# Optimization experiments

Hardware: AMD Instinct MI355X
Metric: run time of the kernel (lower is better)

The kernel has to match this reference:

```python
import jax, jax.numpy as jnp
import numpy as np
from jax import lax

DELTA = 5.0
SCALES = (10.0, 10.0, 10.0)


def _cdiff(v, axis, delta):
    # central difference along `axis` with replicate (edge) padding; output
    # boundary values are discarded later by the interior slice, so the pad
    # mode does not affect the final loss.
    axis = axis % v.ndim
    pad = [(0, 0)] * v.ndim
    pad[axis] = (1, 1)
    vp = jnp.pad(v, pad, mode='edge')
    hi = tuple(slice(2, None) if i == axis else slice(None) for i in range(v.ndim))
    lo = tuple(slice(0, -2) if i == axis else slice(None) for i in range(v.ndim))
    return (vp[hi] - vp[lo]) / (2.0 * delta)


def _vorticity(vel, delta):
    # vel: [N,3,D,H,W] with (u,v,w); x=-1, y=-2, z=-3
    u, v, w = vel[:, 0], vel[:, 1], vel[:, 2]
    vor_x = _cdiff(w, -2, delta) - _cdiff(v, -3, delta)  # dw/dy - dv/dz
    vor_y = _cdiff(u, -3, delta) - _cdiff(w, -1, delta)  # du/dz - dw/dx
    vor_z = _cdiff(v, -1, delta) - _cdiff(u, -2, delta)  # dv/dx - du/dy
    return jnp.stack([vor_x, vor_y, vor_z], axis=1)


def _mask_near_build_wall(building):
    # building: [N,1,D,H,W] binary. 3x3x3 box filter == windowed sum.
    is_in_build = 1.0 - building
    filt = lax.reduce_window(is_in_build, 0.0, lax.add,
                             (1, 1, 3, 3, 3), (1, 1, 1, 1, 1), 'SAME')
    filt = (filt > 0).astype(building.dtype)
    return ((filt * building) > 0).astype(building.dtype)


def _masked_vorticity(bs, preds, scales, delta):
    scl = jnp.asarray(scales, dtype=preds.dtype)
    vel = scl[None, :, None, None, None] * preds[:, 1:]
    omega = _vorticity(vel, delta)
    near = _mask_near_build_wall(bs)
    omega = omega[..., 1:-1, 1:-1, 1:-1]
    b = bs[..., 1:-1, 1:-1, 1:-1]
    nw = near[..., 1:-1, 1:-1, 1:-1]
    omega = omega * b * (1.0 - nw)
    num_grids = jnp.sum(b) - jnp.sum(nw)
    return omega, num_grids


def _safe_norm_ch(d):
    # 2-norm over channel dim with zero (not NaN) grad at d == 0.
    sq = jnp.sum(d * d, axis=1, keepdims=True)
    nz = sq > 0
    return jnp.where(nz, jnp.sqrt(jnp.where(nz, sq, 1.0)), 0.0)


def setup_inputs() -> dict:
    key = jax.random.key(0)
    k1, k2, k3 = jax.random.split(key, 3)
    B, C, D, H, W = 2, 4, 64, 256, 256
    predicts = jax.random.normal(k1, (B, C, D, H, W), dtype=jnp.float32)
    targets = jax.random.normal(k2, (B, C, D, H, W), dtype=jnp.float32)
    masks = jax.random.bernoulli(k3, 0.9, (B, 1, D, H, W)).astype(jnp.float32)
    return {"predicts": predicts, "targets": targets, "masks": masks}


def reference(predicts, targets, masks):
    pred, n1 = _masked_vorticity(masks, predicts, SCALES, DELTA)
    trgt, n2 = _masked_vorticity(masks, targets, SCALES, DELTA)
    diff = _safe_norm_ch(pred - trgt)
    return jnp.sum(diff) / n1
```

## Files before the change

kernel.cpp:

```cpp
#include <hip/hip_runtime.h>


#define SD 65536LL
#define SC 4194304LL

__global__ __launch_bounds__(256) void vort_dense(
    const float* __restrict__ preds, const float* __restrict__ targs,
    const float* __restrict__ masks, double* __restrict__ acc, int slot_mask)
{
    const int lane = threadIdx.x & 63;
    const int wv   = threadIdx.x >> 6;
    int blk = blockIdx.x;
    const int tile = blk & 63; blk >>= 6;
    const int d = blk % 62 + 1; blk /= 62;
    const int b = blk;
    const int h = 1 + tile * 4 + wv;
    const int w0 = lane << 2;

    float norm = 0.0f, cnt = 0.0f;

    if (h <= 254) {
        const long long mbase = (long long)b * SC + (long long)d * SD
                              + (long long)h * 256 + w0;
        const long long b1 = ((long long)(b * 4 + 1) * 64 + d) * SD
                           + (long long)h * 256 + w0;
        const long long b2 = b1 + SC;
        const long long b3 = b2 + SC;

        long long voff[10];
        voff[0] = b1 - SD;  voff[1] = b1 + SD;
        voff[2] = b1 - 256; voff[3] = b1 + 256;
        voff[4] = b2 - SD;  voff[5] = b2 + SD;
        voff[6] = b2;
        voff[7] = b3 - 256; voff[8] = b3 + 256;
        voff[9] = b3;

        float4 P[10], T[10], Mv[9];
        #pragma unroll
        for (int i = 0; i < 10; ++i) P[i] = *(const float4*)(preds + voff[i]);
        #pragma unroll
        for (int i = 0; i < 10; ++i) T[i] = *(const float4*)(targs + voff[i]);
        #pragma unroll
        for (int r = 0; r < 9; ++r) {
            const int dd = r / 3 - 1, dh = r % 3 - 1;
            Mv[r] = *(const float4*)(masks + mbase + (long long)dd * SD
                                     + (long long)dh * 256);
        }

        float Df[10][4];
        #pragma unroll
        for (int i = 0; i < 10; ++i) {
            Df[i][0] = P[i].x - T[i].x; Df[i][1] = P[i].y - T[i].y;
            Df[i][2] = P[i].z - T[i].z; Df[i][3] = P[i].w - T[i].w;
        }
        float4 M = Mv[0];
        #pragma unroll
        for (int r = 1; r < 9; ++r) {
            M.x = fminf(M.x, Mv[r].x); M.y = fminf(M.y, Mv[r].y);
            M.z = fminf(M.z, Mv[r].z); M.w = fminf(M.w, Mv[r].w);
        }

        const float vL = __shfl_up(Df[6][3], 1, 64);
        const float vR = __shfl_down(Df[6][0], 1, 64);
        const float wL = __shfl_up(Df[9][3], 1, 64);
        const float wR = __shfl_down(Df[9][0], 1, 64);
        const float ML = __shfl_up(M.w, 1, 64);
        const float MR = __shfl_down(M.x, 1, 64);

        const float vv[6] = { vL, Df[6][0], Df[6][1], Df[6][2], Df[6][3], vR };
        const float ww[6] = { wL, Df[9][0], Df[9][1], Df[9][2], Df[9][3], wR };
        const float Mm[6] = { ML, M.x, M.y, M.z, M.w, MR };

        #pragma unroll
        for (int j = 0; j < 4; ++j) {
            const int wc = w0 + j;
            const float keepv = fminf(fminf(Mm[j], Mm[j + 1]), Mm[j + 2]);
            const bool valid = (wc >= 1) && (wc <= 254) && (keepv > 0.5f);
            const float wx = (Df[8][j] - Df[7][j]) - (Df[5][j] - Df[4][j]);
            const float wy = (Df[1][j] - Df[0][j]) - (ww[j + 2] - ww[j]);
            const float wz = (vv[j + 2] - vv[j]) - (Df[3][j] - Df[2][j]);
            const float n = sqrtf(wx * wx + wy * wy + wz * wz);
            norm += valid ? n : 0.0f;
            cnt  += valid ? 1.0f : 0.0f;
        }
    }

    #pragma unroll
    for (int off = 32; off > 0; off >>= 1) {
        norm += __shfl_down(norm, off, 64);
        cnt  += __shfl_down(cnt,  off, 64);
    }
    __shared__ float ssum[4], scnt[4];
    if (lane == 0) { ssum[wv] = norm; scnt[wv] = cnt; }
    __syncthreads();
    if (threadIdx.x == 0) {
        const float s = ssum[0] + ssum[1] + ssum[2] + ssum[3];
        const float c = scnt[0] + scnt[1] + scnt[2] + scnt[3];
        double* slot = acc + 2 * (blockIdx.x & slot_mask);
        atomicAdd(&slot[0], (double)s);
        atomicAdd(&slot[1], (double)c);
    }
}

__global__ __launch_bounds__(256) void finalize_kernel(
    const double* __restrict__ acc, float* __restrict__ out, int nslots)
{
    const int lane = threadIdx.x & 63;
    const int wv   = threadIdx.x >> 6;
    double s = 0.0, c = 0.0;
    for (int i = threadIdx.x; i < nslots; i += 256) {
        s += acc[2 * i];
        c += acc[2 * i + 1];
    }
    #pragma unroll
    for (int off = 32; off > 0; off >>= 1) {
        s += __shfl_down(s, off, 64);
        c += __shfl_down(c, off, 64);
    }
    __shared__ double ss[4], sc[4];
    if (lane == 0) { ss[wv] = s; sc[wv] = c; }
    __syncthreads();
    if (threadIdx.x == 0) {
        const double S = ss[0] + ss[1] + ss[2] + ss[3];
        const double C = sc[0] + sc[1] + sc[2] + sc[3];
        out[0] = (C != 0.0) ? (float)(S / C) : 0.0f;
    }
}

extern "C" void kernel_launch(void* const* d_in, const int* in_sizes, int n_in,
                              void* d_out, int out_size, void* d_ws, size_t ws_size,
                              hipStream_t stream)
{
    const float* preds = (const float*)d_in[0];
    const float* targs = (const float*)d_in[1];
    const float* masks = (const float*)d_in[2];
    float* out = (float*)d_out;
    double* acc = (double*)d_ws;

    int nslots = 256;
    while ((size_t)nslots * 2 * sizeof(double) > ws_size && nslots > 1)
        nslots >>= 1;

    hipMemsetAsync(d_ws, 0, (size_t)nslots * 2 * sizeof(double), stream);

    const int nblocks = 2 * 62 * 64;
    vort_dense<<<nblocks, 256, 0, stream>>>(preds, targs, masks, acc,
                                            nslots - 1);
    finalize_kernel<<<1, 256, 0, stream>>>(acc, out, nslots);
}
```

Baseline: 295.5 us.

## March along depth per thread with rolling registers for z-neighbors and masks

Result: faster. 286.8 us (-3.0%).

```diff
diff --git a/kernel.cpp b/kernel.cpp
--- a/kernel.cpp
+++ b/kernel.cpp
@@ -4,7 +4,16 @@
 #define SD 65536LL
 #define SC 4194304LL
 
-__global__ __launch_bounds__(256) void vort_dense(
+__device__ __forceinline__ float4 sub4(float4 a, float4 b) {
+    return make_float4(a.x - b.x, a.y - b.y, a.z - b.z, a.w - b.w);
+}
+__device__ __forceinline__ float4 min4(float4 a, float4 b) {
+    return make_float4(fminf(a.x, b.x), fminf(a.y, b.y),
+                       fminf(a.z, b.z), fminf(a.w, b.w));
+}
+#define C4(v, j) ((j) == 0 ? (v).x : (j) == 1 ? (v).y : (j) == 2 ? (v).z : (v).w)
+
+__global__ __launch_bounds__(256) void vort_march(
     const float* __restrict__ preds, const float* __restrict__ targs,
     const float* __restrict__ masks, double* __restrict__ acc, int slot_mask)
 {
@@ -12,76 +21,100 @@
     const int wv   = threadIdx.x >> 6;
     int blk = blockIdx.x;
     const int tile = blk & 63; blk >>= 6;
-    const int d = blk % 62 + 1; blk /= 62;
-    const int b = blk;
+    const int c    = blk & 15; blk >>= 4;
+    const int b    = blk;
+    const int d0   = 1 + 4 * c;
+    const int nstep = (c < 15) ? 4 : 2;
     const int h = 1 + tile * 4 + wv;
     const int w0 = lane << 2;
 
     float norm = 0.0f, cnt = 0.0f;
 
     if (h <= 254) {
-        const long long mbase = (long long)b * SC + (long long)d * SD
-                              + (long long)h * 256 + w0;
-        const long long b1 = ((long long)(b * 4 + 1) * 64 + d) * SD
-                           + (long long)h * 256 + w0;
-        const long long b2 = b1 + SC;
-        const long long b3 = b2 + SC;
+        const long long rowhw = (long long)h * 256 + w0;
+        const long long mrow  = (long long)b * SC + (long long)d0 * SD + rowhw;
+        const long long urow  = ((long long)(b * 4 + 1) * 64 + d0) * SD + rowhw;
+        const long long vrow  = urow + SC;
+        const long long wrow  = vrow + SC;
 
-        long long voff[10];
-        voff[0] = b1 - SD;  voff[1] = b1 + SD;
-        voff[2] = b1 - 256; voff[3] = b1 + 256;
-        voff[4] = b2 - SD;  voff[5] = b2 + SD;
-        voff[6] = b2;
-        voff[7] = b3 - 256; voff[8] = b3 + 256;
-        voff[9] = b3;
+        float4 Pu0 = *(const float4*)(preds + urow - SD);
+        float4 Pu1 = *(const float4*)(preds + urow);
+        float4 Pv0 = *(const float4*)(preds + vrow - SD);
+        float4 Pv1 = *(const float4*)(preds + vrow);
+        float4 Tu0 = *(const float4*)(targs + urow - SD);
+        float4 Tu1 = *(const float4*)(targs + urow);
+        float4 Tv0 = *(const float4*)(targs + vrow - SD);
+        float4 Tv1 = *(const float4*)(targs + vrow);
+        float4 Ma0 = *(const float4*)(masks + mrow - SD - 256);
+        float4 Mb0 = *(const float4*)(masks + mrow - SD);
+        float4 Mc0 = *(const float4*)(masks + mrow - SD + 256);
+        float4 Ma1 = *(const float4*)(masks + mrow - 256);
+        float4 Mb1 = *(const float4*)(masks + mrow);
+        float4 Mc1 = *(const float4*)(masks + mrow + 256);
 
-        float4 P[10], T[10], Mv[9];
-        #pragma unroll
-        for (int i = 0; i < 10; ++i) P[i] = *(const float4*)(preds + voff[i]);
-        #pragma unroll
-        for (int i = 0; i < 10; ++i) T[i] = *(const float4*)(targs + voff[i]);
-        #pragma unroll
-        for (int r = 0; r < 9; ++r) {
-            const int dd = r / 3 - 1, dh = r % 3 - 1;
-            Mv[r] = *(const float4*)(masks + mbase + (long long)dd * SD
-                                     + (long long)dh * 256);
-        }
+        float4 cu0 = sub4(Pu0, Tu0), cu1 = sub4(Pu1, Tu1);
+        float4 cv0 = sub4(Pv0, Tv0), cv1 = sub4(Pv1, Tv1);
+        float4 m0  = min4(Ma0, min4(Mb0, Mc0));
+        float4 m1  = min4(Ma1, min4(Mb1, Mc1));
 
-        float Df[10][4];
-        #pragma unroll
-        for (int i = 0; i < 10; ++i) {
-            Df[i][0] = P[i].x - T[i].x; Df[i][1] = P[i].y - T[i].y;
-            Df[i][2] = P[i].z - T[i].z; Df[i][3] = P[i].w - T[i].w;
-        }
-        float4 M = Mv[0];
-        #pragma unroll
-        for (int r = 1; r < 9; ++r) {
-            M.x = fminf(M.x, Mv[r].x); M.y = fminf(M.y, Mv[r].y);
-            M.z = fminf(M.z, Mv[r].z); M.w = fminf(M.w, Mv[r].w);
-        }
+        for (int s = 0; s < nstep; ++s) {
+            const long long o = (long long)s * SD;
 
-        const float vL = __shfl_up(Df[6][3], 1, 64);
-        const float vR = __shfl_down(Df[6][0], 1, 64);
-        const float wL = __shfl_up(Df[9][3], 1, 64);
-        const float wR = __shfl_down(Df[9][0], 1, 64);
-        const float ML = __shfl_up(M.w, 1, 64);
-        const float MR = __shfl_down(M.x, 1, 64);
+            float4 PuN  = *(const float4*)(preds + urow + o + SD);
+            float4 Puhm = *(const float4*)(preds + urow + o - 256);
+            float4 Puhp = *(const float4*)(preds + urow + o + 256);
+            float4 PvN  = *(const float4*)(preds + vrow + o + SD);
+            float4 Pwm  = *(const float4*)(preds + wrow + o - 256);
+            float4 Pwc  = *(const float4*)(preds + wrow + o);
+            float4 Pwp  = *(const float4*)(preds + wrow + o + 256);
+            float4 TuN  = *(const float4*)(targs + urow + o + SD);
+            float4 Tuhm = *(const float4*)(targs + urow + o - 256);
+            float4 Tuhp = *(const float4*)(targs + urow + o + 256);
+            float4 TvN  = *(const float4*)(targs + vrow + o + SD);
+            float4 Twm  = *(const float4*)(targs + wrow + o - 256);
+            float4 Twc  = *(const float4*)(targs + wrow + o);
+            float4 Twp  = *(const float4*)(targs + wrow + o + 256);
+            float4 MaN  = *(const float4*)(masks + mrow + o + SD - 256);
+            float4 MbN  = *(const float4*)(masks + mrow + o + SD);
+            float4 McN  = *(const float4*)(masks + mrow + o + SD + 256);
 
-        const float vv[6] = { vL, Df[6][0], Df[6][1], Df[6][2], Df[6][3], vR };
-        const float ww[6] = { wL, Df[9][0], Df[9][1], Df[9][2], Df[9][3], wR };
-        const float Mm[6] = { ML, M.x, M.y, M.z, M.w, MR };
+            float4 cu2 = sub4(PuN, TuN);
+            float4 uhm = sub4(Puhm, Tuhm);
+            float4 uhp = sub4(Puhp, Tuhp);
+            float4 cv2 = sub4(PvN, TvN);
+            float4 wm  = sub4(Pwm, Twm);
+            float4 wc4 = sub4(Pwc, Twc);
+            float4 wp  = sub4(Pwp, Twp);
+            float4 m2  = min4(MaN, min4(MbN, McN));
+            float4 keep4 = min4(m0, min4(m1, m2));
 
-        #pragma unroll
-        for (int j = 0; j < 4; ++j) {
-            const int wc = w0 + j;
-            const float keepv = fminf(fminf(Mm[j], Mm[j + 1]), Mm[j + 2]);
-            const bool valid = (wc >= 1) && (wc <= 254) && (keepv > 0.5f);
-            const float wx = (Df[8][j] - Df[7][j]) - (Df[5][j] - Df[4][j]);
-            const float wy = (Df[1][j] - Df[0][j]) - (ww[j + 2] - ww[j]);
-            const float wz = (vv[j + 2] - vv[j]) - (Df[3][j] - Df[2][j]);
-            const float n = sqrtf(wx * wx + wy * wy + wz * wz);
-            norm += valid ? n : 0.0f;
-            cnt  += valid ? 1.0f : 0.0f;
+            const float vLs = __shfl_up(cv1.w, 1, 64);
+            const float vRs = __shfl_down(cv1.x, 1, 64);
+            const float wLs = __shfl_up(wc4.w, 1, 64);
+            const float wRs = __shfl_down(wc4.x, 1, 64);
+            const float kLs = __shfl_up(keep4.w, 1, 64);
+            const float kRs = __shfl_down(keep4.x, 1, 64);
+
+            const float vv[6] = { vLs, cv1.x, cv1.y, cv1.z, cv1.w, vRs };
+            const float ww[6] = { wLs, wc4.x, wc4.y, wc4.z, wc4.w, wRs };
+            const float kk[6] = { kLs, keep4.x, keep4.y, keep4.z, keep4.w, kRs };
+
+            #pragma unroll
+            for (int j = 0; j < 4; ++j) {
+                const int wcI = w0 + j;
+                const float keep = fminf(fminf(kk[j], kk[j + 1]), kk[j + 2]);
+                const bool valid = (wcI >= 1) && (wcI <= 254) && (keep > 0.5f);
+                const float wx = (C4(wp, j) - C4(wm, j)) - (C4(cv2, j) - C4(cv0, j));
+                const float wy = (C4(cu2, j) - C4(cu0, j)) - (ww[j + 2] - ww[j]);
+                const float wz = (vv[j + 2] - vv[j]) - (C4(uhp, j) - C4(uhm, j));
+                const float n = sqrtf(wx * wx + wy * wy + wz * wz);
+                norm += valid ? n : 0.0f;
+                cnt  += valid ? 1.0f : 0.0f;
+            }
+
+            cu0 = cu1; cu1 = cu2;
+            cv0 = cv1; cv1 = cv2;
+            m0  = m1;  m1  = m2;
         }
     }
 
@@ -95,10 +128,10 @@
     __syncthreads();
     if (threadIdx.x == 0) {
         const float s = ssum[0] + ssum[1] + ssum[2] + ssum[3];
-        const float c = scnt[0] + scnt[1] + scnt[2] + scnt[3];
+        const float c2 = scnt[0] + scnt[1] + scnt[2] + scnt[3];
         double* slot = acc + 2 * (blockIdx.x & slot_mask);
         atomicAdd(&slot[0], (double)s);
-        atomicAdd(&slot[1], (double)c);
+        atomicAdd(&slot[1], (double)c2);
     }
 }
 
@@ -143,8 +176,8 @@
 
     hipMemsetAsync(d_ws, 0, (size_t)nslots * 2 * sizeof(double), stream);
 
-    const int nblocks = 2 * 62 * 64;
-    vort_dense<<<nblocks, 256, 0, stream>>>(preds, targs, masks, acc,
+    const int nblocks = 2 * 16 * 64;
+    vort_march<<<nblocks, 256, 0, stream>>>(preds, targs, masks, acc,
                                             nslots - 1);
     finalize_kernel<<<1, 256, 0, stream>>>(acc, out, nslots);
 }
```
